# Optimization experiments

Hardware: AMD Instinct MI355X
Metric: run time of the kernel (lower is better)

## Reference

```python
import jax, jax.numpy as jnp
import numpy as np

B, D = 8192, 1024
TEMPERATURE = 0.05
NEG_INF = -9e15


def setup_inputs() -> dict:
    key = jax.random.key(0)
    k1, k2, k3 = jax.random.split(key, 3)
    emb = jax.random.normal(k1, (B, D), dtype=jnp.float32)
    # L2-normalize so sim/temperature is numerically sane (as in real usage)
    emb = emb / jnp.linalg.norm(emb, axis=-1, keepdims=True)
    relations = jax.random.randint(k2, (B,), 0, 128, dtype=jnp.int64)
    is_true_samples = jax.random.bernoulli(k3, 0.5, (B,))
    return {"embeddings": emb, "relations": relations, "is_true_samples": is_true_samples}


def reference(embeddings, relations, is_true_samples):
    b = embeddings.shape[0]
    # [B, B] similarity, diagonal masked to -9e15 as in the original
    sim = jnp.matmul(embeddings, embeddings.T) / TEMPERATURE
    eye = jnp.eye(b, dtype=bool)
    sim = jnp.where(eye, NEG_INF, sim)
    # positive_pairs[i, j] = is_true[i] & is_true[j] & (rel[i] == rel[j]) & (i != j)
    pos = (
        (relations[:, None] == relations[None, :])
        & is_true_samples[:, None]
        & is_true_samples[None, :]
        & ~eye
    )
    exp_sim = jnp.exp(sim)                      # diagonal exp(-9e15) -> 0
    sum_exp = exp_sim.sum(axis=1)               # [B]
    numer = jnp.where(pos, exp_sim, 0.0).sum(axis=1)  # [B]
    has_pos = pos.any(axis=1)                   # [B]
    numer_safe = jnp.where(has_pos, numer, 1.0)
    losses = -jnp.log(numer_safe / (sum_exp + 1e-8))
    n_rows = has_pos.sum()
    loss = jnp.where(
        n_rows > 0,
        jnp.where(has_pos, losses, 0.0).sum() / jnp.maximum(n_rows, 1).astype(losses.dtype),
        jnp.asarray(0.0, dtype=losses.dtype),
    )
    num_positives = n_rows  # rows having at least one positive, as in the original
    return loss, num_positives
```

## Files before the change

### kernel.cpp

```cpp
#include <hip/hip_runtime.h>
#include <hip/hip_bf16.h>
#include <hip/hip_fp8.h>
#include <stdint.h>

#define NB 8192
#define ND 1024
#define SCALE 20.0f
#define PRESCALE 16.0f
#define EXPSCALE (SCALE / (PRESCALE * PRESCALE))

typedef __bf16 bf16x8 __attribute__((ext_vector_type(8)));
typedef float  f32x4  __attribute__((ext_vector_type(4)));

__device__ inline void detect_formats(const void* rel_raw, const void* ist_raw,
                                      int& rel64, int& bmode) {
  const unsigned int* r = (const unsigned int*)rel_raw;
  int is64 = 1;
  for (int i = 1; i < 256; i += 2) {
    if (r[i] != 0u) { is64 = 0; break; }
  }
  rel64 = is64;
  const unsigned int* t = (const unsigned int*)ist_raw;
  bool sawf = false, sawbig = false;
  for (int i = 0; i < 64; ++i) {
    unsigned int w = t[i];
    if (w == 0x3F800000u) sawf = true;
    else if (w > 1u) sawbig = true;
  }
  bmode = sawf ? 2 : (sawbig ? 1 : 0);
}

__device__ inline int decode_key(const void* rel_raw, const void* ist_raw,
                                 int rel64, int bmode, int i) {
  const int* r32 = (const int*)rel_raw;
  int r = rel64 ? r32[2 * i] : r32[i];
  int truth;
  if (bmode == 1)      truth = (((const unsigned char*)ist_raw)[i] != 0);
  else if (bmode == 2) truth = (((const float*)ist_raw)[i] != 0.0f);
  else                 truth = (((const int*)ist_raw)[i] != 0);
  return truth ? r : -1;
}

__device__ inline bf16x8 cvt8(const float4& a, const float4& b) {
  bf16x8 v;
  v[0] = (__bf16)a.x; v[1] = (__bf16)a.y; v[2] = (__bf16)a.z; v[3] = (__bf16)a.w;
  v[4] = (__bf16)b.x; v[5] = (__bf16)b.y; v[6] = (__bf16)b.z; v[7] = (__bf16)b.w;
  return v;
}

__device__ inline unsigned long long cvt8f8(const float4& a, const float4& b) {
  float v[8] = {a.x, a.y, a.z, a.w, b.x, b.y, b.z, b.w};
  unsigned long long pk = 0;
#pragma unroll
  for (int i = 0; i < 8; ++i) {
    __hip_fp8_e4m3 h(v[i] * PRESCALE);
    pk |= (unsigned long long)(unsigned char)h.__x << (8 * i);
  }
  return pk;
}

__global__ void prep_kernel(const float* __restrict__ emb,
                            const void* __restrict__ rel_raw,
                            const void* __restrict__ ist_raw,
                            unsigned char* __restrict__ emb8,
                            float* __restrict__ sum_exp,
                            float* __restrict__ numer,
                            int* __restrict__ key) {
  int tid = blockIdx.x * 256 + threadIdx.x;
  size_t base = (size_t)tid * 8;
  if (base < (size_t)NB * ND) {
    float4 a = *(const float4*)(emb + base);
    float4 b = *(const float4*)(emb + base + 4);
    *(unsigned long long*)(emb8 + base) = cvt8f8(a, b);
  }
  if (tid < NB) { sum_exp[tid] = 0.f; numer[tid] = 0.f; }
  __shared__ int s_rel64, s_bmode;
  if (blockIdx.x < 32) {
    if (threadIdx.x == 0) {
      int a, b; detect_formats(rel_raw, ist_raw, a, b);
      s_rel64 = a; s_bmode = b;
    }
    __syncthreads();
    int i = blockIdx.x * 256 + threadIdx.x;
    key[i] = decode_key(rel_raw, ist_raw, s_rel64, s_bmode, i);
  }
}

__global__ void prep_small_kernel(const void* __restrict__ rel_raw,
                                  const void* __restrict__ ist_raw,
                                  float* __restrict__ sum_exp,
                                  float* __restrict__ numer,
                                  int* __restrict__ key) {
  int i = blockIdx.x * 256 + threadIdx.x;
  sum_exp[i] = 0.f; numer[i] = 0.f;
  __shared__ int s_rel64, s_bmode;
  if (threadIdx.x == 0) {
    int a, b; detect_formats(rel_raw, ist_raw, a, b);
    s_rel64 = a; s_bmode = b;
  }
  __syncthreads();
  key[i] = decode_key(rel_raw, ist_raw, s_rel64, s_bmode, i);
}


__global__ __launch_bounds__(256, 4)
void gemm_f8p_kernel(const unsigned char* __restrict__ emb8,
                     const int* __restrict__ key,
                     float* __restrict__ sum_exp,
                     float* __restrict__ numer) {
  __shared__ unsigned char sT[3 * 2 * 4096];
  __shared__ int keyR[128], keyC[128];

  const int bid = blockIdx.x;
  const int t = (bid & 7) * 260 + (bid >> 3);
  int r = (int)((sqrtf(8.f * (float)t + 1.f) - 1.f) * 0.5f);
  while ((r + 1) * (r + 2) / 2 <= t) ++r;
  while (r * (r + 1) / 2 > t) --r;
  const int bx = r, by = t - r * (r + 1) / 2;
  const bool diag = (bx == by);
  const int rowBase = by * 128, colBase = bx * 128;

  const int tid = threadIdx.x;
  const int wid = tid >> 6;
  const int l   = tid & 63;
  const int wr  = wid >> 1;
  const int wc  = wid & 1;
  const int fragOff = ((l & 15) << 5) + ((((l >> 5) & 1) ^ ((l >> 2) & 1)) << 4)
                    + (((l >> 4) & 1) << 3);
  const int sband = l >> 5;
  const int srow  = (l >> 1) & 15;
  const int scol  = (((l & 1) ^ ((srow >> 2) & 1)) << 4);

  if (tid < 128) keyR[tid] = key[rowBase + tid];
  else           keyC[tid - 128] = key[colBase + tid - 128];
  asm volatile("" ::: "memory");

  const size_t rowOff = (size_t)(rowBase + (wid * 2 + sband) * 16 + srow) * ND + scol;
  const size_t colOff = (size_t)(colBase + (wid * 2 + sband) * 16 + srow) * ND + scol;

  __builtin_amdgcn_global_load_lds(
      (const __attribute__((address_space(1))) void*)(emb8 + rowOff),
      (__attribute__((address_space(3))) void*)&sT[0 * 8192 + 0 + wid * 1024], 16, 0, 0);
  __builtin_amdgcn_global_load_lds(
      (const __attribute__((address_space(1))) void*)(emb8 + colOff),
      (__attribute__((address_space(3))) void*)&sT[0 * 8192 + 4096 + wid * 1024], 16, 0, 0);

  f32x4 acc[4][4] = {};
  int rb = 0, wb = 1;

#pragma unroll 1
  for (int kt = 0; kt < 32; ++kt) {
    if (kt < 31) {
      int k0 = (kt + 1) * 32;
      __builtin_amdgcn_global_load_lds(
          (const __attribute__((address_space(1))) void*)(emb8 + rowOff + k0),
          (__attribute__((address_space(3))) void*)&sT[wb * 8192 + 0 + wid * 1024], 16, 0, 0);
      __builtin_amdgcn_global_load_lds(
          (const __attribute__((address_space(1))) void*)(emb8 + colOff + k0),
          (__attribute__((address_space(3))) void*)&sT[wb * 8192 + 4096 + wid * 1024], 16, 0, 0);
      asm volatile("s_waitcnt vmcnt(2) lgkmcnt(0)" ::: "memory");
    } else {
      asm volatile("s_waitcnt vmcnt(0) lgkmcnt(0)" ::: "memory");
    }
    __builtin_amdgcn_s_barrier();
    asm volatile("" ::: "memory");

    const unsigned char* cA = &sT[rb * 8192];
    const unsigned char* cB = &sT[rb * 8192 + 4096];
    long af[4], bfr[4];
#pragma unroll
    for (int m = 0; m < 4; ++m)
      af[m] = *(const long*)&cA[((wr * 4 + m) << 9) + fragOff];
#pragma unroll
    for (int n = 0; n < 4; ++n)
      bfr[n] = *(const long*)&cB[((wc * 4 + n) << 9) + fragOff];
#pragma unroll
    for (int m = 0; m < 4; ++m)
#pragma unroll
      for (int n = 0; n < 4; ++n)
        acc[m][n] = __builtin_amdgcn_mfma_f32_16x16x32_fp8_fp8(af[m], bfr[n], acc[m][n], 0, 0, 0);

    rb = (rb == 2) ? 0 : rb + 1;
    wb = (wb == 2) ? 0 : wb + 1;
  }

  float cse[4] = {0.f, 0.f, 0.f, 0.f};
  float cnu[4] = {0.f, 0.f, 0.f, 0.f};
#pragma unroll
  for (int m = 0; m < 4; ++m) {
#pragma unroll
    for (int r4 = 0; r4 < 4; ++r4) {
      int li = wr * 64 + m * 16 + (l >> 4) * 4 + r4;
      int gi = rowBase + li;
      int krow = keyR[li];
      float se = 0.f, nu = 0.f;
#pragma unroll
      for (int n = 0; n < 4; ++n) {
        int lj = wc * 64 + n * 16 + (l & 15);
        int gj = colBase + lj;
        float e = __expf(acc[m][n][r4] * EXPSCALE);
        if (gi == gj) e = 0.f;
        bool match = (krow >= 0) && (krow == keyC[lj]);
        se += e;
        if (match) nu += e;
        if (!diag) {
          cse[n] += e;
          if (match) cnu[n] += e;
        }
      }
#pragma unroll
      for (int off = 8; off; off >>= 1) {
        se += __shfl_xor(se, off, 16);
        nu += __shfl_xor(nu, off, 16);
      }
      if ((l & 15) == 0) {
        atomicAdd(&sum_exp[gi], se);
        if (nu != 0.f) atomicAdd(&numer[gi], nu);
      }
    }
  }
  if (!diag) {
#pragma unroll
    for (int n = 0; n < 4; ++n) {
      cse[n] += __shfl_xor(cse[n], 16);
      cse[n] += __shfl_xor(cse[n], 32);
      cnu[n] += __shfl_xor(cnu[n], 16);
      cnu[n] += __shfl_xor(cnu[n], 32);
    }
    if (l < 16) {
#pragma unroll
      for (int n = 0; n < 4; ++n) {
        int gj = colBase + wc * 64 + n * 16 + l;
        atomicAdd(&sum_exp[gj], cse[n]);
        if (cnu[n] != 0.f) atomicAdd(&numer[gj], cnu[n]);
      }
    }
  }
}

__global__ __launch_bounds__(256, 4)
void gemm_fused_f32_kernel(const float* __restrict__ embF,
                           const int* __restrict__ key,
                           float* __restrict__ sum_exp,
                           float* __restrict__ numer) {
  __shared__ __bf16 sA[128 * 64];
  __shared__ __bf16 sB[128 * 64];
  __shared__ int keyR[128], keyC[128];

  const int t = blockIdx.x;
  int r = (int)((sqrtf(8.f * (float)t + 1.f) - 1.f) * 0.5f);
  while ((r + 1) * (r + 2) / 2 <= t) ++r;
  while (r * (r + 1) / 2 > t) --r;
  const int bx = r;
  const int by = t - r * (r + 1) / 2;
  const bool diag = (bx == by);

  const int tid = threadIdx.x;
  const int wid = tid >> 6;
  const int l   = tid & 63;
  const int wr  = wid >> 1;
  const int wc  = wid & 1;
  const int rowBase = by * 128;
  const int colBase = bx * 128;

  if (tid < 128) keyR[tid] = key[rowBase + tid];
  else           keyC[tid - 128] = key[colBase + tid - 128];

  f32x4 acc[4][4] = {};

  for (int k0 = 0; k0 < ND; k0 += 64) {
    __syncthreads();
#pragma unroll
    for (int c = 0; c < 4; ++c) {
      int chunk = tid + c * 256;
      int row = chunk >> 3;
      int ko  = (chunk & 7) * 8;
      const float* gfa = embF + (size_t)(rowBase + row) * ND + k0 + ko;
      const float* gfb = embF + (size_t)(colBase + row) * ND + k0 + ko;
      float4 a0 = *(const float4*)gfa;
      float4 a1 = *(const float4*)(gfa + 4);
      float4 b0 = *(const float4*)gfb;
      float4 b1 = *(const float4*)(gfb + 4);
      *(bf16x8*)&sA[row * 64 + ko] = cvt8(a0, a1);
      *(bf16x8*)&sB[row * 64 + ko] = cvt8(b0, b1);
    }
    __syncthreads();

#pragma unroll
    for (int kk = 0; kk < 2; ++kk) {
      bf16x8 af[4], bfr[4];
#pragma unroll
      for (int m = 0; m < 4; ++m)
        af[m] = *(const bf16x8*)&sA[(wr * 64 + m * 16 + (l & 15)) * 64 + kk * 32 + (l >> 4) * 8];
#pragma unroll
      for (int n = 0; n < 4; ++n)
        bfr[n] = *(const bf16x8*)&sB[(wc * 64 + n * 16 + (l & 15)) * 64 + kk * 32 + (l >> 4) * 8];
#pragma unroll
      for (int m = 0; m < 4; ++m)
#pragma unroll
        for (int n = 0; n < 4; ++n)
          acc[m][n] = __builtin_amdgcn_mfma_f32_16x16x32_bf16(af[m], bfr[n], acc[m][n], 0, 0, 0);
    }
  }

  float cse[4] = {0.f, 0.f, 0.f, 0.f};
  float cnu[4] = {0.f, 0.f, 0.f, 0.f};
#pragma unroll
  for (int m = 0; m < 4; ++m) {
#pragma unroll
    for (int r4 = 0; r4 < 4; ++r4) {
      int li = wr * 64 + m * 16 + (l >> 4) * 4 + r4;
      int gi = rowBase + li;
      int krow = keyR[li];
      float se = 0.f, nu = 0.f;
#pragma unroll
      for (int n = 0; n < 4; ++n) {
        int lj = wc * 64 + n * 16 + (l & 15);
        int gj = colBase + lj;
        float e = __expf(acc[m][n][r4] * SCALE);
        if (gi == gj) e = 0.f;
        bool match = (krow >= 0) && (krow == keyC[lj]);
        se += e;
        if (match) nu += e;
        if (!diag) {
          cse[n] += e;
          if (match) cnu[n] += e;
        }
      }
#pragma unroll
      for (int off = 8; off; off >>= 1) {
        se += __shfl_xor(se, off, 16);
        nu += __shfl_xor(nu, off, 16);
      }
      if ((l & 15) == 0) {
        atomicAdd(&sum_exp[gi], se);
        if (nu != 0.f) atomicAdd(&numer[gi], nu);
      }
    }
  }
  if (!diag) {
#pragma unroll
    for (int n = 0; n < 4; ++n) {
      cse[n] += __shfl_xor(cse[n], 16);
      cse[n] += __shfl_xor(cse[n], 32);
      cnu[n] += __shfl_xor(cnu[n], 16);
      cnu[n] += __shfl_xor(cnu[n], 32);
    }
    if (l < 16) {
#pragma unroll
      for (int n = 0; n < 4; ++n) {
        int gj = colBase + wc * 64 + n * 16 + l;
        atomicAdd(&sum_exp[gj], cse[n]);
        if (cnu[n] != 0.f) atomicAdd(&numer[gj], cnu[n]);
      }
    }
  }
}

__global__ void finalize_kernel(const float* __restrict__ sum_exp,
                                const float* __restrict__ numer,
                                const int* __restrict__ key,
                                float* __restrict__ out) {
  __shared__ int cnt[128];
  __shared__ float wsum[16];
  __shared__ int wcnt[16];
  int tid = threadIdx.x;
  if (tid < 128) cnt[tid] = 0;
  __syncthreads();
  for (int i = tid; i < NB; i += 1024) {
    int k = key[i];
    if (k >= 0) atomicAdd(&cnt[k], 1);
  }
  __syncthreads();
  float ls = 0.f; int np = 0;
  for (int i = tid; i < NB; i += 1024) {
    int k = key[i];
    if (k >= 0 && cnt[k] >= 2) {
      np++;
      ls += logf(sum_exp[i] + 1e-8f) - logf(numer[i]);
    }
  }
  for (int off = 32; off; off >>= 1) {
    ls += __shfl_down(ls, off, 64);
    np += __shfl_down(np, off, 64);
  }
  int w = tid >> 6;
  if ((tid & 63) == 0) { wsum[w] = ls; wcnt[w] = np; }
  __syncthreads();
  if (tid == 0) {
    float s = 0.f; int n = 0;
    for (int i = 0; i < 16; ++i) { s += wsum[i]; n += wcnt[i]; }
    out[0] = (n > 0) ? (s / (float)n) : 0.f;
    out[1] = (float)n;
  }
}

#define NT128 64
#define NTRI128 (NT128 * (NT128 + 1) / 2)

extern "C" void kernel_launch(void* const* d_in, const int* in_sizes, int n_in,
                              void* d_out, int out_size, void* d_ws, size_t ws_size,
                              hipStream_t stream) {
  const float* emb = (const float*)d_in[0];
  const void* rel  = d_in[1];
  const void* ist  = d_in[2];
  float* out = (float*)d_out;

  const size_t emb8Bytes = (size_t)NB * ND;
  const size_t smallBytes = (size_t)NB * 4 * 3;

  char* ws = (char*)d_ws;
  if (ws_size >= emb8Bytes + smallBytes) {
    unsigned char* emb8 = (unsigned char*)ws;
    float* sum_exp = (float*)(ws + emb8Bytes);
    float* numer   = sum_exp + NB;
    int*   key     = (int*)(numer + NB);
    prep_kernel<<<4096, 256, 0, stream>>>(emb, rel, ist, emb8, sum_exp, numer, key);
    gemm_f8p_kernel<<<NTRI128, 256, 0, stream>>>(emb8, key, sum_exp, numer);
    finalize_kernel<<<1, 1024, 0, stream>>>(sum_exp, numer, key, out);
  } else {
    float* sum_exp = (float*)ws;
    float* numer   = sum_exp + NB;
    int*   key     = (int*)(numer + NB);
    prep_small_kernel<<<32, 256, 0, stream>>>(rel, ist, sum_exp, numer, key);
    gemm_fused_f32_kernel<<<NTRI128, 256, 0, stream>>>(emb, key, sum_exp, numer);
    finalize_kernel<<<1, 1024, 0, stream>>>(sum_exp, numer, key, out);
  }
}
```

Before: 115.7 us.

## Double the K-step per stage in FP8 GEMM with new LDS swizzle and setprio

The FP8 similarity GEMM now loads a 64-wide K slice per pipeline stage instead of 32, which halves the number of loop iterations and barriers. Each stage issues four async global-to-LDS loads. The LDS tile uses a new XOR swizzle with 64-byte rows, and each stage runs two MFMA sub-steps wrapped in s_setprio to favour matrix issue. The LDS footprint doubles to 48KB per block, which may reduce occupancy under launch_bounds(256,4).

Result: faster. 103.2 us (-10.8%).

```diff
diff --git a/kernel.cpp b/kernel.cpp
--- a/kernel.cpp
+++ b/kernel.cpp
@@ -104,11 +104,11 @@
 
 
 __global__ __launch_bounds__(256, 4)
-void gemm_f8p_kernel(const unsigned char* __restrict__ emb8,
+void gemm_f8w_kernel(const unsigned char* __restrict__ emb8,
                      const int* __restrict__ key,
                      float* __restrict__ sum_exp,
                      float* __restrict__ numer) {
-  __shared__ unsigned char sT[3 * 2 * 4096];
+  __shared__ unsigned char sT[3][2][8192];
   __shared__ int keyR[128], keyC[128];
 
   const int bid = blockIdx.x;
@@ -125,64 +125,94 @@
   const int l   = tid & 63;
   const int wr  = wid >> 1;
   const int wc  = wid & 1;
-  const int fragOff = ((l & 15) << 5) + ((((l >> 5) & 1) ^ ((l >> 2) & 1)) << 4)
-                    + (((l >> 4) & 1) << 3);
-  const int sband = l >> 5;
-  const int srow  = (l >> 1) & 15;
-  const int scol  = (((l & 1) ^ ((srow >> 2) & 1)) << 4);
+
+  const int row = l & 15;
+  const int ks  = l >> 4;
+  const int X   = ((row >> 1) & 3) << 1;
+  const int rd0 = row * 64 + ((ks) ^ X) * 8;
+  const int rd1 = row * 64 + ((4 + ks) ^ X) * 8;
+
+  const int srow = l >> 2;
+  const int Xs   = ((srow >> 1) & 3) << 1;
+  const int scol = ((2 * (l & 3)) ^ Xs) * 8;
 
   if (tid < 128) keyR[tid] = key[rowBase + tid];
   else           keyC[tid - 128] = key[colBase + tid - 128];
   asm volatile("" ::: "memory");
 
-  const size_t rowOff = (size_t)(rowBase + (wid * 2 + sband) * 16 + srow) * ND + scol;
-  const size_t colOff = (size_t)(colBase + (wid * 2 + sband) * 16 + srow) * ND + scol;
-
-  __builtin_amdgcn_global_load_lds(
-      (const __attribute__((address_space(1))) void*)(emb8 + rowOff),
-      (__attribute__((address_space(3))) void*)&sT[0 * 8192 + 0 + wid * 1024], 16, 0, 0);
-  __builtin_amdgcn_global_load_lds(
-      (const __attribute__((address_space(1))) void*)(emb8 + colOff),
-      (__attribute__((address_space(3))) void*)&sT[0 * 8192 + 4096 + wid * 1024], 16, 0, 0);
+  const size_t aOff0 = (size_t)(rowBase + (wid * 2 + 0) * 16 + srow) * ND + scol;
+  const size_t aOff1 = (size_t)(rowBase + (wid * 2 + 1) * 16 + srow) * ND + scol;
+  const size_t bOff0 = (size_t)(colBase + (wid * 2 + 0) * 16 + srow) * ND + scol;
+  const size_t bOff1 = (size_t)(colBase + (wid * 2 + 1) * 16 + srow) * ND + scol;
+  const int dst0 = (wid * 2 + 0) * 1024 + l * 16;
+  const int dst1 = (wid * 2 + 1) * 1024 + l * 16;
+
+#define STAGE(buf, k0)                                                         \
+  do {                                                                         \
+    __builtin_amdgcn_global_load_lds(                                          \
+        (const __attribute__((address_space(1))) void*)(emb8 + aOff0 + (k0)),  \
+        (__attribute__((address_space(3))) void*)&sT[buf][0][dst0], 16, 0, 0); \
+    __builtin_amdgcn_global_load_lds(                                          \
+        (const __attribute__((address_space(1))) void*)(emb8 + aOff1 + (k0)),  \
+        (__attribute__((address_space(3))) void*)&sT[buf][0][dst1], 16, 0, 0); \
+    __builtin_amdgcn_global_load_lds(                                          \
+        (const __attribute__((address_space(1))) void*)(emb8 + bOff0 + (k0)),  \
+        (__attribute__((address_space(3))) void*)&sT[buf][1][dst0], 16, 0, 0); \
+    __builtin_amdgcn_global_load_lds(                                          \
+        (const __attribute__((address_space(1))) void*)(emb8 + bOff1 + (k0)),  \
+        (__attribute__((address_space(3))) void*)&sT[buf][1][dst1], 16, 0, 0); \
+  } while (0)
+
+  STAGE(0, 0);
 
   f32x4 acc[4][4] = {};
   int rb = 0, wb = 1;
 
 #pragma unroll 1
-  for (int kt = 0; kt < 32; ++kt) {
-    if (kt < 31) {
-      int k0 = (kt + 1) * 32;
-      __builtin_amdgcn_global_load_lds(
-          (const __attribute__((address_space(1))) void*)(emb8 + rowOff + k0),
-          (__attribute__((address_space(3))) void*)&sT[wb * 8192 + 0 + wid * 1024], 16, 0, 0);
-      __builtin_amdgcn_global_load_lds(
-          (const __attribute__((address_space(1))) void*)(emb8 + colOff + k0),
-          (__attribute__((address_space(3))) void*)&sT[wb * 8192 + 4096 + wid * 1024], 16, 0, 0);
-      asm volatile("s_waitcnt vmcnt(2) lgkmcnt(0)" ::: "memory");
+  for (int kt = 0; kt < 16; ++kt) {
+    if (kt < 15) {
+      STAGE(wb, (kt + 1) * 64);
+      asm volatile("s_waitcnt vmcnt(4) lgkmcnt(0)" ::: "memory");
     } else {
       asm volatile("s_waitcnt vmcnt(0) lgkmcnt(0)" ::: "memory");
     }
     __builtin_amdgcn_s_barrier();
     asm volatile("" ::: "memory");
 
-    const unsigned char* cA = &sT[rb * 8192];
-    const unsigned char* cB = &sT[rb * 8192 + 4096];
+    const unsigned char* cA = &sT[rb][0][0];
+    const unsigned char* cB = &sT[rb][1][0];
     long af[4], bfr[4];
 #pragma unroll
     for (int m = 0; m < 4; ++m)
-      af[m] = *(const long*)&cA[((wr * 4 + m) << 9) + fragOff];
+      af[m] = *(const long*)&cA[(wr * 4 + m) * 1024 + rd0];
 #pragma unroll
     for (int n = 0; n < 4; ++n)
-      bfr[n] = *(const long*)&cB[((wc * 4 + n) << 9) + fragOff];
+      bfr[n] = *(const long*)&cB[(wc * 4 + n) * 1024 + rd0];
+    __builtin_amdgcn_s_setprio(1);
 #pragma unroll
     for (int m = 0; m < 4; ++m)
 #pragma unroll
       for (int n = 0; n < 4; ++n)
         acc[m][n] = __builtin_amdgcn_mfma_f32_16x16x32_fp8_fp8(af[m], bfr[n], acc[m][n], 0, 0, 0);
+    __builtin_amdgcn_s_setprio(0);
+#pragma unroll
+    for (int m = 0; m < 4; ++m)
+      af[m] = *(const long*)&cA[(wr * 4 + m) * 1024 + rd1];
+#pragma unroll
+    for (int n = 0; n < 4; ++n)
+      bfr[n] = *(const long*)&cB[(wc * 4 + n) * 1024 + rd1];
+    __builtin_amdgcn_s_setprio(1);
+#pragma unroll
+    for (int m = 0; m < 4; ++m)
+#pragma unroll
+      for (int n = 0; n < 4; ++n)
+        acc[m][n] = __builtin_amdgcn_mfma_f32_16x16x32_fp8_fp8(af[m], bfr[n], acc[m][n], 0, 0, 0);
+    __builtin_amdgcn_s_setprio(0);
 
     rb = (rb == 2) ? 0 : rb + 1;
     wb = (wb == 2) ? 0 : wb + 1;
   }
+#undef STAGE
 
   float cse[4] = {0.f, 0.f, 0.f, 0.f};
   float cnu[4] = {0.f, 0.f, 0.f, 0.f};
@@ -416,7 +446,7 @@
     float* numer   = sum_exp + NB;
     int*   key     = (int*)(numer + NB);
     prep_kernel<<<4096, 256, 0, stream>>>(emb, rel, ist, emb8, sum_exp, numer, key);
-    gemm_f8p_kernel<<<NTRI128, 256, 0, stream>>>(emb8, key, sum_exp, numer);
+    gemm_f8w_kernel<<<NTRI128, 256, 0, stream>>>(emb8, key, sum_exp, numer);
     finalize_kernel<<<1, 1024, 0, stream>>>(sum_exp, numer, key, out);
   } else {
     float* sum_exp = (float*)ws;
```
